# Performance work log

Measured on AMD Instinct MI355X. Metric: run time of the kernel, lower is better.

## Reference

```python
import jax, jax.numpy as jnp
import numpy as np

B, C_MAX, T = 128, 272, 512
D1 = 320
NUM_SUBJECTS = 8
NUM_CHANNELS = [272, 256, 240, 224, 208, 270, 260, 248]


def setup_inputs() -> dict:
    key = jax.random.key(0)
    k_x, k_w, k_s = jax.random.split(key, 3)
    X = jax.random.normal(k_x, (B, C_MAX, T), dtype=jnp.float32)
    subject_idxs = jax.random.randint(k_s, (B,), 0, NUM_SUBJECTS)
    # Per-subject Conv1d(kernel=1, bias=False) weights, padded to C_MAX.
    # Original module only reads the first num_channels[s] input channels;
    # zeroing the padded columns reproduces that exactly.
    W = jax.random.normal(k_w, (NUM_SUBJECTS, D1, C_MAX), dtype=jnp.float32) * 0.02
    mask = np.zeros((NUM_SUBJECTS, 1, C_MAX), dtype=np.float32)
    for s, nc in enumerate(NUM_CHANNELS):
        mask[s, 0, :nc] = 1.0
    W = W * jnp.asarray(mask)
    return {"X": X, "subject_idxs": subject_idxs, "W": W}


def reference(X, subject_idxs, W):
    # Gather per-sample weight matrix [B, D1, C_MAX] by subject id, then
    # batched 1x1 conv == matmul over channels at every time step.
    Wsel = W[subject_idxs]                      # [B, D1, C]
    out = jnp.einsum("bdc,bct->bdt", Wsel, X)   # [B, D1, T]
    return out
```

## Files before the change

kernel.cpp:

```cpp
#include <hip/hip_runtime.h>

#define BB    128
#define CC    272
#define TT    512
#define DD1   320
#define KC    32
#define NCHUNK 9
#define NT    64
#define MT    160
#define LDA   40
#define LDBT  40

typedef float  f32x4  __attribute__((ext_vector_type(4)));
typedef __bf16 bf16x4 __attribute__((ext_vector_type(4)));
typedef __bf16 bf16x8 __attribute__((ext_vector_type(8)));

#define BAR() asm volatile("s_waitcnt lgkmcnt(0)\ns_barrier" ::: "memory")

__global__ __launch_bounds__(256, 4)
void subj_conv_mfma(const float* __restrict__ X,
                    const int*   __restrict__ sidx,
                    const float* __restrict__ W,
                    float*       __restrict__ out) {
    const int b  = blockIdx.x;
    const int T0 = blockIdx.y * NT;
    const int d0 = blockIdx.z * MT;
    const int s  = sidx[b];

    __shared__ __align__(16) __bf16 As[2][MT * LDA];
    __shared__ __align__(16) __bf16 Bs[2][NT * LDBT];

    const int tid  = threadIdx.x;
    const int lane = tid & 63;
    const int wv   = tid >> 6;
    const int wm   = wv & 1;
    const int wn   = wv >> 1;
    const int quad = lane >> 4;
    const int l16  = lane & 15;

    const float* Wb = W + ((size_t)s * DD1 + d0) * CC;
    const float* Xb = X + (size_t)b * CC * TT + T0;

    const int am  = tid >> 3;
    const int akk = (tid & 7) * 4;
    const float* Xc = Xb + (size_t)(8 * wv) * TT + lane;

    f32x4 acc[5][2];
#pragma unroll
    for (int mt = 0; mt < 5; ++mt) {
        acc[mt][0] = (f32x4){0.f, 0.f, 0.f, 0.f};
        acc[mt][1] = (f32x4){0.f, 0.f, 0.f, 0.f};
    }

    float4 pa[5];
    float  pbx[8];

    auto load_chunk_full = [&](int c0) {
#pragma unroll
        for (int p = 0; p < 5; ++p)
            pa[p] = *(const float4*)(Wb + (size_t)(am + 32 * p) * CC + c0 + akk);
#pragma unroll
        for (int r = 0; r < 8; ++r)
            pbx[r] = Xc[(size_t)(c0 + r) * TT];
    };

    auto load_chunk_guard = [&](int c0) {
#pragma unroll
        for (int p = 0; p < 5; ++p) {
            const int c = c0 + akk;
            float4 v = make_float4(0.f, 0.f, 0.f, 0.f);
            if (c < CC) v = *(const float4*)(Wb + (size_t)(am + 32 * p) * CC + c);
            pa[p] = v;
        }
#pragma unroll
        for (int r = 0; r < 8; ++r) {
            const int c = c0 + 8 * wv + r;
            pbx[r] = (c < CC) ? Xc[(size_t)(c0 + r) * TT] : 0.f;
        }
    };

    auto store_chunk = [&](int buf) {
#pragma unroll
        for (int p = 0; p < 5; ++p) {
            bf16x4 h = {(__bf16)pa[p].x, (__bf16)pa[p].y,
                        (__bf16)pa[p].z, (__bf16)pa[p].w};
            *(bf16x4*)&As[buf][(am + 32 * p) * LDA + akk] = h;
        }
        bf16x8 hb;
#pragma unroll
        for (int r = 0; r < 8; ++r) hb[r] = (__bf16)pbx[r];
        *(bf16x8*)&Bs[buf][lane * LDBT + 8 * wv] = hb;
    };

    load_chunk_full(0);
    store_chunk(0);
    load_chunk_full(KC);
    BAR();

    for (int kc = 0; kc < NCHUNK; ++kc) {
        const int cur = kc & 1;

        bf16x8 bfr[2];
#pragma unroll
        for (int nt = 0; nt < 2; ++nt)
            bfr[nt] = *(const bf16x8*)&Bs[cur][(wn * 32 + nt * 16 + l16) * LDBT + quad * 8];

#pragma unroll
        for (int mt = 0; mt < 5; ++mt) {
            bf16x8 af = *(const bf16x8*)&As[cur][(wm * 80 + mt * 16 + l16) * LDA + quad * 8];
#pragma unroll
            for (int nt = 0; nt < 2; ++nt)
                acc[mt][nt] = __builtin_amdgcn_mfma_f32_16x16x32_bf16(
                    af, bfr[nt], acc[mt][nt], 0, 0, 0);
        }

        if (kc + 1 < NCHUNK) {
            store_chunk(1 - cur);
            if (kc + 2 < NCHUNK) {
                const int c0 = (kc + 2) * KC;
                if (kc + 2 == NCHUNK - 1) load_chunk_guard(c0);
                else                      load_chunk_full(c0);
            }
            BAR();
        }
    }

#pragma unroll
    for (int mt = 0; mt < 5; ++mt) {
        const int d = d0 + wm * 80 + mt * 16 + quad * 4;
#pragma unroll
        for (int nt = 0; nt < 2; ++nt) {
            float* ob = out + ((size_t)b * DD1 + d) * TT + T0 + wn * 32 + nt * 16 + l16;
#pragma unroll
            for (int r = 0; r < 4; ++r)
                ob[(size_t)r * TT] = acc[mt][nt][r];
        }
    }
}

extern "C" void kernel_launch(void* const* d_in, const int* in_sizes, int n_in,
                              void* d_out, int out_size, void* d_ws, size_t ws_size,
                              hipStream_t stream) {
    const float* X    = (const float*)d_in[0];
    const int*   sidx = (const int*)  d_in[1];
    const float* W    = (const float*)d_in[2];
    float*       out  = (float*)d_out;

    dim3 grid(BB, TT / NT, 2);
    dim3 block(256);
    subj_conv_mfma<<<grid, block, 0, stream>>>(X, sidx, W, out);
}
```

Measured before the change: 184.2 us.

## Deepen register prefetch to two chunks and swizzle block order for locality

Global loads are staged through two register sets, so chunks are prefetched two iterations ahead while the LDS stays double-buffered, and the loop is fully unrolled. The grid is flattened to 1D and remapped so consecutive blocks cover 8 batches across all 16 tiles, aiming to improve L2 reuse of the X and W slices. Occupancy is lowered from 4 to 3 blocks per CU to make room for the extra prefetch registers. This trades some latency hiding from wave parallelism for deeper per-wave load pipelining.

```diff
diff --git a/kernel.cpp b/kernel.cpp
--- a/kernel.cpp
+++ b/kernel.cpp
@@ -17,15 +17,17 @@
 
 #define BAR() asm volatile("s_waitcnt lgkmcnt(0)\ns_barrier" ::: "memory")
 
-__global__ __launch_bounds__(256, 4)
+__global__ __launch_bounds__(256, 3)
 void subj_conv_mfma(const float* __restrict__ X,
                     const int*   __restrict__ sidx,
                     const float* __restrict__ W,
                     float*       __restrict__ out) {
-    const int b  = blockIdx.x;
-    const int T0 = blockIdx.y * NT;
-    const int d0 = blockIdx.z * MT;
-    const int s  = sidx[b];
+    const int bid  = blockIdx.x;
+    const int b    = (bid & 7) + 8 * (bid >> 7);
+    const int tile = (bid >> 3) & 15;
+    const int T0   = (tile >> 1) * NT;
+    const int d0   = (tile & 1) * MT;
+    const int s    = sidx[b];
 
     __shared__ __align__(16) __bf16 As[2][MT * LDA];
     __shared__ __align__(16) __bf16 Bs[2][NT * LDBT];
@@ -52,10 +54,10 @@
         acc[mt][1] = (f32x4){0.f, 0.f, 0.f, 0.f};
     }
 
-    float4 pa[5];
-    float  pbx[8];
+    float4 pa0[5], pa1[5];
+    float  pb0[8], pb1[8];
 
-    auto load_chunk_full = [&](int c0) {
+    auto load_full = [&](float4 (&pa)[5], float (&pbx)[8], int c0) {
 #pragma unroll
         for (int p = 0; p < 5; ++p)
             pa[p] = *(const float4*)(Wb + (size_t)(am + 32 * p) * CC + c0 + akk);
@@ -64,7 +66,7 @@
             pbx[r] = Xc[(size_t)(c0 + r) * TT];
     };
 
-    auto load_chunk_guard = [&](int c0) {
+    auto load_guard = [&](float4 (&pa)[5], float (&pbx)[8], int c0) {
 #pragma unroll
         for (int p = 0; p < 5; ++p) {
             const int c = c0 + akk;
@@ -79,7 +81,7 @@
         }
     };
 
-    auto store_chunk = [&](int buf) {
+    auto store_chunk = [&](int buf, const float4 (&pa)[5], const float (&pbx)[8]) {
 #pragma unroll
         for (int p = 0; p < 5; ++p) {
             bf16x4 h = {(__bf16)pa[p].x, (__bf16)pa[p].y,
@@ -92,19 +94,11 @@
         *(bf16x8*)&Bs[buf][lane * LDBT + 8 * wv] = hb;
     };
 
-    load_chunk_full(0);
-    store_chunk(0);
-    load_chunk_full(KC);
-    BAR();
-
-    for (int kc = 0; kc < NCHUNK; ++kc) {
-        const int cur = kc & 1;
-
+    auto compute = [&](int cur) {
         bf16x8 bfr[2];
 #pragma unroll
         for (int nt = 0; nt < 2; ++nt)
             bfr[nt] = *(const bf16x8*)&Bs[cur][(wn * 32 + nt * 16 + l16) * LDBT + quad * 8];
-
 #pragma unroll
         for (int mt = 0; mt < 5; ++mt) {
             bf16x8 af = *(const bf16x8*)&As[cur][(wm * 80 + mt * 16 + l16) * LDA + quad * 8];
@@ -113,17 +107,34 @@
                 acc[mt][nt] = __builtin_amdgcn_mfma_f32_16x16x32_bf16(
                     af, bfr[nt], acc[mt][nt], 0, 0, 0);
         }
+    };
 
-        if (kc + 1 < NCHUNK) {
-            store_chunk(1 - cur);
-            if (kc + 2 < NCHUNK) {
-                const int c0 = (kc + 2) * KC;
-                if (kc + 2 == NCHUNK - 1) load_chunk_guard(c0);
-                else                      load_chunk_full(c0);
+    load_full(pa0, pb0, 0);
+    load_full(pa1, pb1, KC);
+    store_chunk(0, pa0, pb0);
+    load_full(pa0, pb0, 2 * KC);
+    BAR();
+
+#pragma unroll
+    for (int kc = 0; kc < 8; kc += 2) {
+        compute(0);
+        store_chunk(1, pa1, pb1);
+        if (kc + 3 < NCHUNK) {
+            if (kc + 3 == NCHUNK - 1) load_guard(pa1, pb1, (kc + 3) * KC);
+            else                      load_full (pa1, pb1, (kc + 3) * KC);
+        }
+        BAR();
+        compute(1);
+        if (kc + 2 < NCHUNK) {
+            store_chunk(0, pa0, pb0);
+            if (kc + 4 < NCHUNK) {
+                if (kc + 4 == NCHUNK - 1) load_guard(pa0, pb0, (kc + 4) * KC);
+                else                      load_full (pa0, pb0, (kc + 4) * KC);
             }
             BAR();
         }
     }
+    compute(0);
 
 #pragma unroll
     for (int mt = 0; mt < 5; ++mt) {
@@ -146,7 +157,7 @@
     const float* W    = (const float*)d_in[2];
     float*       out  = (float*)d_out;
 
-    dim3 grid(BB, TT / NT, 2);
+    dim3 grid(BB * (TT / NT) * 2);
     dim3 block(256);
     subj_conv_mfma<<<grid, block, 0, stream>>>(X, sidx, W, out);
 }
```

Result: no change. 181.1 us (-1.7%).

## Stage full X tile in LDS once, read bf16 W directly from global

Applied to the files above, without the earlier changes.

Loads the block's whole 272x64 X tile into LDS as bf16 in one pass with a single barrier, replacing the double-buffered chunk pipeline. W fragments are read straight from global memory into MFMA operands. When workspace is available, a pre-pass kernel converts W to bf16 so each fragment is a single 16-byte load. This removes per-chunk barriers and LDS staging of W. In exchange it adds an extra kernel launch, scalar strided LDS reads for the B fragments, and uncoalesced global W loads that rely on the cache.

```diff
diff --git a/kernel.cpp b/kernel.cpp
--- a/kernel.cpp
+++ b/kernel.cpp
@@ -2,33 +2,41 @@
 
 #define BB    128
 #define CC    272
+#define CPAD  288
 #define TT    512
 #define DD1   320
-#define KC    32
-#define NCHUNK 9
 #define NT    64
 #define MT    160
-#define LDA   40
-#define LDBT  40
+#define LDC   66
 
 typedef float  f32x4  __attribute__((ext_vector_type(4)));
 typedef __bf16 bf16x4 __attribute__((ext_vector_type(4)));
 typedef __bf16 bf16x8 __attribute__((ext_vector_type(8)));
 
-#define BAR() asm volatile("s_waitcnt lgkmcnt(0)\ns_barrier" ::: "memory")
+__global__ __launch_bounds__(256)
+void w_cvt(const float* __restrict__ W, __bf16* __restrict__ Wb) {
+    const int i = blockIdx.x * 256 + threadIdx.x;
+    const float4* src = (const float4*)W;
+    const float4 a = src[2 * i];
+    const float4 b = src[2 * i + 1];
+    bf16x8 h = {(__bf16)a.x, (__bf16)a.y, (__bf16)a.z, (__bf16)a.w,
+                (__bf16)b.x, (__bf16)b.y, (__bf16)b.z, (__bf16)b.w};
+    *(bf16x8*)(Wb + 8 * i) = h;
+}
 
+template <bool WB16>
 __global__ __launch_bounds__(256, 4)
-void subj_conv_mfma(const float* __restrict__ X,
-                    const int*   __restrict__ sidx,
-                    const float* __restrict__ W,
-                    float*       __restrict__ out) {
+void subj_conv_mfma(const float*  __restrict__ X,
+                    const int*    __restrict__ sidx,
+                    const float*  __restrict__ W,
+                    const __bf16* __restrict__ Wbf,
+                    float*        __restrict__ out) {
     const int b  = blockIdx.x;
     const int T0 = blockIdx.y * NT;
     const int d0 = blockIdx.z * MT;
     const int s  = sidx[b];
 
-    __shared__ __align__(16) __bf16 As[2][MT * LDA];
-    __shared__ __align__(16) __bf16 Bs[2][NT * LDBT];
+    __shared__ __align__(16) __bf16 Xs[CPAD * LDC];
 
     const int tid  = threadIdx.x;
     const int lane = tid & 63;
@@ -38,12 +46,28 @@
     const int quad = lane >> 4;
     const int l16  = lane & 15;
 
-    const float* Wb = W + ((size_t)s * DD1 + d0) * CC;
     const float* Xb = X + (size_t)b * CC * TT + T0;
 
-    const int am  = tid >> 3;
-    const int akk = (tid & 7) * 4;
-    const float* Xc = Xb + (size_t)(8 * wv) * TT + lane;
+    const int xr = tid >> 4;
+    const int xt = (tid & 15) * 4;
+#pragma unroll
+    for (int pb = 0; pb < 3; ++pb) {
+        float4 v[6];
+#pragma unroll
+        for (int q = 0; q < 6; ++q) {
+            const int c = xr + 16 * (pb * 6 + q);
+            v[q] = make_float4(0.f, 0.f, 0.f, 0.f);
+            if (c < CC) v[q] = *(const float4*)(Xb + (size_t)c * TT + xt);
+        }
+#pragma unroll
+        for (int q = 0; q < 6; ++q) {
+            const int c = xr + 16 * (pb * 6 + q);
+            bf16x4 h = {(__bf16)v[q].x, (__bf16)v[q].y,
+                        (__bf16)v[q].z, (__bf16)v[q].w};
+            *(bf16x4*)&Xs[c * LDC + xt] = h;
+        }
+    }
+    __syncthreads();
 
     f32x4 acc[5][2];
 #pragma unroll
@@ -52,76 +76,39 @@
         acc[mt][1] = (f32x4){0.f, 0.f, 0.f, 0.f};
     }
 
-    float4 pa[5];
-    float  pbx[8];
+    const int tc0 = wn * 32 + l16;
+    const int tc1 = tc0 + 16;
+    const size_t wrow = ((size_t)s * DD1 + d0 + wm * 80 + l16) * CC + quad * 8;
+    const __bf16* Wp16 = Wbf + (WB16 ? wrow : 0);
+    const float*  Wp32 = W   + (WB16 ? 0 : wrow);
 
-    auto load_chunk_full = [&](int c0) {
 #pragma unroll
-        for (int p = 0; p < 5; ++p)
-            pa[p] = *(const float4*)(Wb + (size_t)(am + 32 * p) * CC + c0 + akk);
+    for (int kc = 0; kc < 9; ++kc) {
+        bf16x8 b0, b1;
 #pragma unroll
-        for (int r = 0; r < 8; ++r)
-            pbx[r] = Xc[(size_t)(c0 + r) * TT];
-    };
-
-    auto load_chunk_guard = [&](int c0) {
-#pragma unroll
-        for (int p = 0; p < 5; ++p) {
-            const int c = c0 + akk;
-            float4 v = make_float4(0.f, 0.f, 0.f, 0.f);
-            if (c < CC) v = *(const float4*)(Wb + (size_t)(am + 32 * p) * CC + c);
-            pa[p] = v;
+        for (int j = 0; j < 8; ++j) {
+            const int crow = (kc * 32 + quad * 8 + j) * LDC;
+            b0[j] = Xs[crow + tc0];
+            b1[j] = Xs[crow + tc1];
         }
 #pragma unroll
-        for (int r = 0; r < 8; ++r) {
-            const int c = c0 + 8 * wv + r;
-            pbx[r] = (c < CC) ? Xc[(size_t)(c0 + r) * TT] : 0.f;
-        }
-    };
-
-    auto store_chunk = [&](int buf) {
-#pragma unroll
-        for (int p = 0; p < 5; ++p) {
-            bf16x4 h = {(__bf16)pa[p].x, (__bf16)pa[p].y,
-                        (__bf16)pa[p].z, (__bf16)pa[p].w};
-            *(bf16x4*)&As[buf][(am + 32 * p) * LDA + akk] = h;
-        }
-        bf16x8 hb;
-#pragma unroll
-        for (int r = 0; r < 8; ++r) hb[r] = (__bf16)pbx[r];
-        *(bf16x8*)&Bs[buf][lane * LDBT + 8 * wv] = hb;
-    };
-
-    load_chunk_full(0);
-    store_chunk(0);
-    load_chunk_full(KC);
-    BAR();
-
-    for (int kc = 0; kc < NCHUNK; ++kc) {
-        const int cur = kc & 1;
-
-        bf16x8 bfr[2];
-#pragma unroll
-        for (int nt = 0; nt < 2; ++nt)
-            bfr[nt] = *(const bf16x8*)&Bs[cur][(wn * 32 + nt * 16 + l16) * LDBT + quad * 8];
-
-#pragma unroll
         for (int mt = 0; mt < 5; ++mt) {
-            bf16x8 af = *(const bf16x8*)&As[cur][(wm * 80 + mt * 16 + l16) * LDA + quad * 8];
-#pragma unroll
-            for (int nt = 0; nt < 2; ++nt)
-                acc[mt][nt] = __builtin_amdgcn_mfma_f32_16x16x32_bf16(
-                    af, bfr[nt], acc[mt][nt], 0, 0, 0);
-        }
-
-        if (kc + 1 < NCHUNK) {
-            store_chunk(1 - cur);
-            if (kc + 2 < NCHUNK) {
-                const int c0 = (kc + 2) * KC;
-                if (kc + 2 == NCHUNK - 1) load_chunk_guard(c0);
-                else                      load_chunk_full(c0);
+            const int off = mt * 16 * CC + kc * 32;
+            bf16x8 af = {(__bf16)0.f, (__bf16)0.f, (__bf16)0.f, (__bf16)0.f,
+                         (__bf16)0.f, (__bf16)0.f, (__bf16)0.f, (__bf16)0.f};
+            const bool live = (kc < 8) || (quad < 2);
+            if (live) {
+                if constexpr (WB16) {
+                    af = *(const bf16x8*)(Wp16 + off);
+                } else {
+                    const float4 u0 = *(const float4*)(Wp32 + off);
+                    const float4 u1 = *(const float4*)(Wp32 + off + 4);
+                    af = bf16x8{(__bf16)u0.x, (__bf16)u0.y, (__bf16)u0.z, (__bf16)u0.w,
+                                (__bf16)u1.x, (__bf16)u1.y, (__bf16)u1.z, (__bf16)u1.w};
+                }
             }
-            BAR();
+            acc[mt][0] = __builtin_amdgcn_mfma_f32_16x16x32_bf16(af, b0, acc[mt][0], 0, 0, 0);
+            acc[mt][1] = __builtin_amdgcn_mfma_f32_16x16x32_bf16(af, b1, acc[mt][1], 0, 0, 0);
         }
     }
 
@@ -148,5 +135,13 @@
 
     dim3 grid(BB, TT / NT, 2);
     dim3 block(256);
-    subj_conv_mfma<<<grid, block, 0, stream>>>(X, sidx, W, out);
+
+    const size_t need = (size_t)8 * DD1 * CC * sizeof(__bf16);
+    if (d_ws && ws_size >= need) {
+        __bf16* Wb = (__bf16*)d_ws;
+        w_cvt<<<dim3(340), dim3(256), 0, stream>>>(W, Wb);
+        subj_conv_mfma<true><<<grid, block, 0, stream>>>(X, sidx, W, Wb, out);
+    } else {
+        subj_conv_mfma<false><<<grid, block, 0, stream>>>(X, sidx, W, nullptr, out);
+    }
 }
```

Measured after the change: 167.9 us. 1.1x faster.
